# Optimization experiments

Measured on AMD Instinct MI355X. Metric: run time of the kernel, lower is better.

## Reference

```python
import jax, jax.numpy as jnp
import numpy as np

N_IN = 4096      # input features
N_NPB = 64       # neurons (inputs) per branch column
N_B = 64         # branches
N_NEXT_H = 256   # next hidden width
COLS = N_B * N_NEXT_H
BATCH = 128


def setup_inputs() -> dict:
    key = jax.random.key(0)
    k1, k2, k3 = jax.random.split(key, 3)
    x = jax.random.normal(k1, (BATCH, N_IN), dtype=jnp.float32)
    # torch kaiming_normal_ on (n_npb, cols): fan_in = cols, gain = sqrt(2)
    std = np.sqrt(2.0 / COLS).astype(np.float32)
    w = jax.random.normal(k2, (N_NPB, COLS), dtype=jnp.float32) * std
    # random per-column input indices (the module's all_branch_indices)
    idx = jax.random.randint(k3, (N_NPB, COLS), 0, N_IN, dtype=jnp.int32)
    return {"x": x, "w": w, "idx": idx}


def _last_write_mask(idx):
    # (row, col) targets. keep[k, c] is True iff no k' > k has idx[k', c] == idx[k, c].
    eq = idx[:, None, :] == idx[None, :, :]                    # [K, K, C]
    later = jnp.triu(jnp.ones((N_NPB, N_NPB), bool), 1)        # k' > k
    return ~jnp.any(eq & later[:, :, None], axis=1)            # [K, C]


def reference(x, w, idx):
    keep = _last_write_mask(idx)
    w_eff = jnp.where(keep, w, jnp.zeros((), x.dtype))         # [K, C]
    cols = jnp.broadcast_to(jnp.arange(COLS), (N_NPB, COLS))
    # scatter weights into dense [n_in, cols] (equals torch's clone+index_put)
    dense = jnp.zeros((N_IN, COLS), x.dtype).at[idx, cols].add(w_eff)
    out = x @ dense                                            # [B, COLS]
    return out.reshape(-1, N_B, N_NEXT_H)
```

## Files before the change

kernel.cpp:

```cpp
#include <hip/hip_runtime.h>

#define N_IN   4096
#define N_NPB  64
#define COLS   16384
#define BATCH  128

typedef unsigned int       uint;
typedef unsigned short     ushort;
typedef __attribute__((ext_vector_type(2))) _Float16 h2;


static __device__ __forceinline__ ushort f16bits(float v) {
  return __builtin_bit_cast(ushort, (_Float16)v);
}

template <int KB>
static __device__ __forceinline__ void keep_pk(
    const int* __restrict__ ip, const float* __restrict__ wp,
    uint* __restrict__ pkout) {
  int  g[16];
  uint m[16];
#pragma unroll
  for (int j = 0; j < 16; ++j) { g[j] = ip[(KB + j) * COLS]; m[j] = 0xffffffffu; }
#pragma unroll
  for (int j = 0; j < 16; ++j)
#pragma unroll
    for (int kp = j + 1; kp < 16; ++kp)
      m[j] = min(m[j], (uint)(g[j] ^ g[kp]));
#pragma unroll 4
  for (int kp = KB + 16; kp < 64; ++kp) {
    const int vk = ip[kp * COLS];
#pragma unroll
    for (int j = 0; j < 16; ++j) m[j] = min(m[j], (uint)(g[j] ^ vk));
  }
#pragma unroll
  for (int j = 0; j < 16; ++j) {
    const float wv = (m[j] != 0u) ? wp[(KB + j) * COLS] : 0.0f;
    pkout[(KB + j) * COLS] = ((uint)g[j] << 16) | (uint)f16bits(wv);
  }
}

__global__ __launch_bounds__(256, 4) void prep_kernel(
    const float* __restrict__ x, const int* __restrict__ idx,
    const float* __restrict__ w, ushort* __restrict__ xT4,
    uint* __restrict__ pku) {
  const int bid = blockIdx.x;
  const int tid = threadIdx.x;
  if (bid < 512) {
    __shared__ float tile[32][33];
    const int i0 = (bid & 127) * 32;
    const int b0 = (bid >> 7) * 32;
    const int tx = tid & 31;
    const int ty = tid >> 5;
#pragma unroll
    for (int j = 0; j < 32; j += 8)
      tile[ty + j][tx] = x[(b0 + ty + j) * N_IN + i0 + tx];
    __syncthreads();
#pragma unroll
    for (int j = 0; j < 32; j += 8) {
      const int b = b0 + tx, i = i0 + ty + j;
      xT4[((b >> 2) << 14) + (i << 2) + (b & 3)] = f16bits(tile[tx][ty + j]);
    }
  } else {
    const int kg = __builtin_amdgcn_readfirstlane(tid >> 6);
    const int c  = (bid - 512) * 64 + (tid & 63);
    if      (kg == 0) keep_pk<0 >(idx + c, w + c, pku + c);
    else if (kg == 1) keep_pk<16>(idx + c, w + c, pku + c);
    else if (kg == 2) keep_pk<32>(idx + c, w + c, pku + c);
    else              keep_pk<48>(idx + c, w + c, pku + c);
  }
}

__global__ __launch_bounds__(512, 8) void gather_kernel(
    const uint* __restrict__ pku, const ushort* __restrict__ xT4,
    float* __restrict__ out) {
  __shared__ __align__(16) ushort xls[4096 * 4];

  const int tid  = threadIdx.x;
  const int bid  = blockIdx.x;
  const int r    = bid & 31;
  const int s    = bid >> 5;
  const int wave = tid >> 6;
  const int lane = tid & 63;
  const int c    = r * 512 + wave * 64 + lane;

  {
    const ushort* src = xT4 + (s << 14);
#pragma unroll
    for (int t = 0; t < 4; ++t) {
      const int ub = (t * 8 + wave) * 512;
      __builtin_amdgcn_global_load_lds(
          (const __attribute__((address_space(1))) void*)(src + ub + lane * 8),
          (__attribute__((address_space(3))) void*)(xls + ub), 16, 0, 0);
    }
  }
  __syncthreads();

  const uint* pc = pku + c;
  const char* xb = (const char*)xls;
  h2 a0 = (h2)0.0f, a1 = (h2)0.0f, a2 = (h2)0.0f, a3 = (h2)0.0f;
#pragma unroll
  for (int k = 0; k < N_NPB; k += 2) {
    const uint e0 = pc[k * COLS];
    const uint e1 = pc[(k + 1) * COLS];
    const uint o0 = (e0 >> 16) << 3;
    const uint o1 = (e1 >> 16) << 3;
    const uint w0 = e0 & 0xffffu, w1 = e1 & 0xffffu;
    const h2 wh0 = __builtin_bit_cast(h2, (w0 << 16) | w0);
    const h2 wh1 = __builtin_bit_cast(h2, (w1 << 16) | w1);
    const uint2 u0 = *(const uint2*)(xb + o0);
    const uint2 u1 = *(const uint2*)(xb + o1);
    a0 += __builtin_bit_cast(h2, u0.x) * wh0;
    a1 += __builtin_bit_cast(h2, u0.y) * wh0;
    a2 += __builtin_bit_cast(h2, u1.x) * wh1;
    a3 += __builtin_bit_cast(h2, u1.y) * wh1;
  }

  out[(s * 4 + 0) * COLS + c] = (float)a0.x + (float)a2.x;
  out[(s * 4 + 1) * COLS + c] = (float)a0.y + (float)a2.y;
  out[(s * 4 + 2) * COLS + c] = (float)a1.x + (float)a3.x;
  out[(s * 4 + 3) * COLS + c] = (float)a1.y + (float)a3.y;
}

extern "C" void kernel_launch(void* const* d_in, const int* in_sizes, int n_in,
                              void* d_out, int out_size, void* d_ws, size_t ws_size,
                              hipStream_t stream) {
  const float* x   = (const float*)d_in[0];
  const float* w   = (const float*)d_in[1];
  const int*   idx = (const int*)d_in[2];
  float* out = (float*)d_out;

  char* ws = (char*)d_ws;
  ushort* xT4 = (ushort*)(ws);
  uint*   pku = (uint*)(ws + (1u << 20));

  hipLaunchKernelGGL(prep_kernel, dim3(768), dim3(256), 0, stream,
                     x, idx, w, xT4, pku);
  hipLaunchKernelGGL(gather_kernel, dim3(1024), dim3(512), 0, stream,
                     pku, xT4, out);
}
```

Measured before the change: 26.66 us.

## Split K across two gather strategies and combine partial sums with atomics

The main kernel now splits the 64 weight rows into two halves. Even blocks handle rows 0-31 by gathering directly from a new global batch-major fp16 copy of x (xTh), one column group per block with a 16-byte batch vector per lane. Odd blocks handle rows 32-63 with the original LDS-staged path. Both halves accumulate into out with float atomicAdd, so the prep kernel now also zeroes the output. The aim is to halve per-block LDS staging and balance L2-gather against LDS work, at the cost of an extra transposed copy of x, output zeroing, and 2x atomic traffic on the output.

```diff
diff --git a/kernel.cpp b/kernel.cpp
--- a/kernel.cpp
+++ b/kernel.cpp
@@ -7,6 +7,7 @@
 
 typedef unsigned int       uint;
 typedef unsigned short     ushort;
+typedef unsigned long long u64;
 typedef __attribute__((ext_vector_type(2))) _Float16 h2;
 
 
@@ -42,8 +43,9 @@
 
 __global__ __launch_bounds__(256, 4) void prep_kernel(
     const float* __restrict__ x, const int* __restrict__ idx,
-    const float* __restrict__ w, ushort* __restrict__ xT4,
-    uint* __restrict__ pku) {
+    const float* __restrict__ w, ushort* __restrict__ xTh,
+    ushort* __restrict__ xT4, uint* __restrict__ pku,
+    float4* __restrict__ out4) {
   const int bid = blockIdx.x;
   const int tid = threadIdx.x;
   if (bid < 512) {
@@ -59,67 +61,127 @@
 #pragma unroll
     for (int j = 0; j < 32; j += 8) {
       const int b = b0 + tx, i = i0 + ty + j;
-      xT4[((b >> 2) << 14) + (i << 2) + (b & 3)] = f16bits(tile[tx][ty + j]);
-    }
-  } else {
+      const ushort hv = f16bits(tile[tx][ty + j]);
+      xTh[i * BATCH + b] = hv;
+      xT4[((b >> 2) << 14) + (i << 2) + (b & 3)] = hv;
+    }
+  } else if (bid < 768) {
     const int kg = __builtin_amdgcn_readfirstlane(tid >> 6);
     const int c  = (bid - 512) * 64 + (tid & 63);
     if      (kg == 0) keep_pk<0 >(idx + c, w + c, pku + c);
     else if (kg == 1) keep_pk<16>(idx + c, w + c, pku + c);
     else if (kg == 2) keep_pk<32>(idx + c, w + c, pku + c);
     else              keep_pk<48>(idx + c, w + c, pku + c);
-  }
-}
-
-__global__ __launch_bounds__(512, 8) void gather_kernel(
-    const uint* __restrict__ pku, const ushort* __restrict__ xT4,
-    float* __restrict__ out) {
-  __shared__ __align__(16) ushort xls[4096 * 4];
-
-  const int tid  = threadIdx.x;
-  const int bid  = blockIdx.x;
-  const int r    = bid & 31;
-  const int s    = bid >> 5;
-  const int wave = tid >> 6;
-  const int lane = tid & 63;
-  const int c    = r * 512 + wave * 64 + lane;
-
-  {
-    const ushort* src = xT4 + (s << 14);
-#pragma unroll
-    for (int t = 0; t < 4; ++t) {
-      const int ub = (t * 8 + wave) * 512;
-      __builtin_amdgcn_global_load_lds(
-          (const __attribute__((address_space(1))) void*)(src + ub + lane * 8),
-          (__attribute__((address_space(3))) void*)(xls + ub), 16, 0, 0);
-    }
-  }
-  __syncthreads();
-
-  const uint* pc = pku + c;
-  const char* xb = (const char*)xls;
-  h2 a0 = (h2)0.0f, a1 = (h2)0.0f, a2 = (h2)0.0f, a3 = (h2)0.0f;
-#pragma unroll
-  for (int k = 0; k < N_NPB; k += 2) {
-    const uint e0 = pc[k * COLS];
-    const uint e1 = pc[(k + 1) * COLS];
-    const uint o0 = (e0 >> 16) << 3;
-    const uint o1 = (e1 >> 16) << 3;
-    const uint w0 = e0 & 0xffffu, w1 = e1 & 0xffffu;
-    const h2 wh0 = __builtin_bit_cast(h2, (w0 << 16) | w0);
-    const h2 wh1 = __builtin_bit_cast(h2, (w1 << 16) | w1);
-    const uint2 u0 = *(const uint2*)(xb + o0);
-    const uint2 u1 = *(const uint2*)(xb + o1);
-    a0 += __builtin_bit_cast(h2, u0.x) * wh0;
-    a1 += __builtin_bit_cast(h2, u0.y) * wh0;
-    a2 += __builtin_bit_cast(h2, u1.x) * wh1;
-    a3 += __builtin_bit_cast(h2, u1.y) * wh1;
-  }
-
-  out[(s * 4 + 0) * COLS + c] = (float)a0.x + (float)a2.x;
-  out[(s * 4 + 1) * COLS + c] = (float)a0.y + (float)a2.y;
-  out[(s * 4 + 2) * COLS + c] = (float)a1.x + (float)a3.x;
-  out[(s * 4 + 3) * COLS + c] = (float)a1.y + (float)a3.y;
+  } else {
+    const int z = bid - 768;
+    float4 zv; zv.x = zv.y = zv.z = zv.w = 0.0f;
+    for (int i = tid; i < 2048; i += 256) out4[z * 2048 + i] = zv;
+  }
+}
+
+__global__ __launch_bounds__(512, 8) void main_kernel(
+    const uint* __restrict__ pku, const ushort* __restrict__ xTh,
+    const ushort* __restrict__ xT4, float* __restrict__ out) {
+  __shared__ __align__(16) char smem[33024];
+
+  const int bid = blockIdx.x;
+  const int tid = threadIdx.x;
+
+  if ((bid & 1) == 0) {
+    u64   (*pk)[16]       = reinterpret_cast<u64(*)[16]>(smem);
+    float (*res)[16][132] = reinterpret_cast<float(*)[16][132]>(smem + 4096);
+    const int c0 = (bid >> 1) * 16;
+
+    {
+      const int cl = tid & 15, k = tid >> 4;
+      const uint e  = pku[k * COLS + c0 + cl];
+      const uint wb = e & 0xffffu;
+      pk[k][cl] = ((u64)((wb << 16) | wb) << 32) | (u64)((e >> 16) << 8);
+    }
+    __syncthreads();
+
+    const int wave  = tid >> 6;
+    const int khalf = wave >> 2;
+    const int lane  = tid & 63;
+    const int g     = lane >> 4;
+    const int b8    = lane & 15;
+    const int cl    = (wave & 3) * 4 + g;
+
+    const char* xb = (const char*)xTh;
+    const uint  bo = (uint)b8 * 16;
+    const int   kb = khalf * 16;
+
+    h2 a0 = (h2)0.0f, a1 = (h2)0.0f, a2 = (h2)0.0f, a3 = (h2)0.0f;
+#pragma unroll
+    for (int kk = 0; kk < 16; ++kk) {
+      const u64  e   = pk[kb + kk][cl];
+      const uint off = (uint)e + bo;
+      const h2   wh  = __builtin_bit_cast(h2, (uint)(e >> 32));
+      const uint4 u  = *(const uint4*)(xb + off);
+      a0 += __builtin_bit_cast(h2, u.x) * wh;
+      a1 += __builtin_bit_cast(h2, u.y) * wh;
+      a2 += __builtin_bit_cast(h2, u.z) * wh;
+      a3 += __builtin_bit_cast(h2, u.w) * wh;
+    }
+    {
+      float* r = &res[khalf][cl][b8 * 8];
+      r[0] = (float)a0.x; r[1] = (float)a0.y;
+      r[2] = (float)a1.x; r[3] = (float)a1.y;
+      r[4] = (float)a2.x; r[5] = (float)a2.y;
+      r[6] = (float)a3.x; r[7] = (float)a3.y;
+    }
+    __syncthreads();
+
+    for (int e2 = tid; e2 < BATCH * 16; e2 += 512) {
+      const int b = e2 >> 4, cc = e2 & 15;
+      atomicAdd(&out[b * COLS + c0 + cc], res[0][cc][b] + res[1][cc][b]);
+    }
+  } else {
+    ushort* xls = reinterpret_cast<ushort*>(smem);
+    const int b2   = bid >> 1;
+    const int r    = b2 & 31;
+    const int s    = b2 >> 5;
+    const int wave = tid >> 6;
+    const int lane = tid & 63;
+    const int c    = r * 512 + wave * 64 + lane;
+
+    {
+      const ushort* src = xT4 + (s << 14);
+#pragma unroll
+      for (int t = 0; t < 4; ++t) {
+        const int ub = (t * 8 + wave) * 512;
+        __builtin_amdgcn_global_load_lds(
+            (const __attribute__((address_space(1))) void*)(src + ub + lane * 8),
+            (__attribute__((address_space(3))) void*)(xls + ub), 16, 0, 0);
+      }
+    }
+    __syncthreads();
+
+    const uint* pc = pku + 32 * COLS + c;
+    const char* xb = (const char*)xls;
+    h2 a0 = (h2)0.0f, a1 = (h2)0.0f, a2 = (h2)0.0f, a3 = (h2)0.0f;
+#pragma unroll
+    for (int k = 0; k < 32; k += 2) {
+      const uint e0 = pc[k * COLS];
+      const uint e1 = pc[(k + 1) * COLS];
+      const uint o0 = (e0 >> 16) << 3;
+      const uint o1 = (e1 >> 16) << 3;
+      const uint w0 = e0 & 0xffffu, w1 = e1 & 0xffffu;
+      const h2 wh0 = __builtin_bit_cast(h2, (w0 << 16) | w0);
+      const h2 wh1 = __builtin_bit_cast(h2, (w1 << 16) | w1);
+      const uint2 u0 = *(const uint2*)(xb + o0);
+      const uint2 u1 = *(const uint2*)(xb + o1);
+      a0 += __builtin_bit_cast(h2, u0.x) * wh0;
+      a1 += __builtin_bit_cast(h2, u0.y) * wh0;
+      a2 += __builtin_bit_cast(h2, u1.x) * wh1;
+      a3 += __builtin_bit_cast(h2, u1.y) * wh1;
+    }
+
+    atomicAdd(&out[(s * 4 + 0) * COLS + c], (float)a0.x + (float)a2.x);
+    atomicAdd(&out[(s * 4 + 1) * COLS + c], (float)a0.y + (float)a2.y);
+    atomicAdd(&out[(s * 4 + 2) * COLS + c], (float)a1.x + (float)a3.x);
+    atomicAdd(&out[(s * 4 + 3) * COLS + c], (float)a1.y + (float)a3.y);
+  }
 }
 
 extern "C" void kernel_launch(void* const* d_in, const int* in_sizes, int n_in,
@@ -131,11 +193,12 @@
   float* out = (float*)d_out;
 
   char* ws = (char*)d_ws;
-  ushort* xT4 = (ushort*)(ws);
-  uint*   pku = (uint*)(ws + (1u << 20));
-
-  hipLaunchKernelGGL(prep_kernel, dim3(768), dim3(256), 0, stream,
-                     x, idx, w, xT4, pku);
-  hipLaunchKernelGGL(gather_kernel, dim3(1024), dim3(512), 0, stream,
-                     pku, xT4, out);
-}
+  ushort* xTh = (ushort*)(ws);
+  ushort* xT4 = (ushort*)(ws + (1u << 20));
+  uint*   pku = (uint*)(ws + (2u << 20));
+
+  hipLaunchKernelGGL(prep_kernel, dim3(1024), dim3(256), 0, stream,
+                     x, idx, w, xTh, xT4, pku, (float4*)out);
+  hipLaunchKernelGGL(main_kernel, dim3(2048), dim3(512), 0, stream,
+                     pku, xTh, xT4, out);
+}
```

Result: slower. 37.11 us (+39.2%).
